# Optimization experiments

Hardware: AMD Instinct MI355X
Metric: run time of the kernel (lower is better)

Reference implementation:

```python
import jax, jax.numpy as jnp
import numpy as np

S_Q = 2048; B = 2; H = 16; D = 128
SCALE = 1.0 / np.sqrt(128.0)  # softmax_scale from init


def setup_inputs() -> dict:
    key = jax.random.key(0)
    kq, kk, kv, ks = jax.random.split(key, 4)
    q = jax.random.normal(kq, (S_Q, B, H, D), dtype=jnp.float32)
    k = jax.random.normal(kk, (S_Q, B, 1, D), dtype=jnp.float32)   # MQA: H_kv=1
    v = jax.random.normal(kv, (S_Q, B, 1, D), dtype=jnp.float32)
    sinks = jax.random.normal(ks, (H,), dtype=jnp.float32)         # learned per-head sink logits
    return {"q": q, "k": k, "v": v, "sinks": sinks, "mask": 0}


def reference(q, k, v, sinks, mask):
    # q: [S_q, B, H, D]; k, v: [S_k, B, H_kv, D] (H_kv may be 1 -> MQA expand)
    S_q, Bn, Hq, Dn = q.shape
    S_k = k.shape[0]
    k = jnp.broadcast_to(k, (S_k, Bn, Hq, Dn))
    v = jnp.broadcast_to(v, (S_k, Bn, Hq, Dn))
    # logits: [B, H, S_q, S_k]
    logits = jnp.einsum("sbhd,tbhd->bhst", q.astype(jnp.float32), k.astype(jnp.float32)) * SCALE
    # causal mask (triu(-inf, diag=1) added in original)
    causal = jnp.tril(jnp.ones((S_q, S_k), dtype=bool))
    logits = jnp.where(causal[None, None], logits, -jnp.inf)
    # sink-augmented softmax: append sink logit as extra column, softmax, drop it
    sink = sinks.astype(jnp.float32)[None, :, None, None]        # [1, H, 1, 1]
    m = jax.lax.stop_gradient(jnp.maximum(logits.max(axis=-1, keepdims=True), sink))
    e = jnp.exp(logits - m)                                      # [B, H, S_q, S_k]
    denom = e.sum(axis=-1, keepdims=True) + jnp.exp(sink - m)    # sink column contribution
    probs = e / denom
    out = jnp.einsum("bhst,tbhd->sbhd", probs.astype(v.dtype), v)  # [S_q, B, H, D]
    return out.reshape(S_q, Bn, Hq * Dn)
```

## Files before the change

kernel.cpp:

```cpp
#include <hip/hip_runtime.h>

#define SQ 2048
#define NB 2
#define NH 16
#define DH 128
#define NKT 32
#define NQT 32
#define SCALE_L2E 0.1275174609f
#define LOG2E 1.4426950408889634f
#define DEFER_THR 11.0f

typedef _Float16 f16x8 __attribute__((ext_vector_type(8)));
typedef _Float16 f16x4 __attribute__((ext_vector_type(4)));
typedef float f32x4 __attribute__((ext_vector_type(4)));

static __device__ __forceinline__ _Float16 f2h(float f) { return (_Float16)f; }

__global__ __launch_bounds__(256)
void prepack(const float* __restrict__ k, const float* __restrict__ v,
             _Float16* __restrict__ kws, _Float16* __restrict__ vws) {
    const int bid   = blockIdx.x;
    const int which = bid >> 6;
    const int b     = (bid >> 5) & 1;
    const int t     = bid & 31;
    const int tid   = threadIdx.x;

    if (which == 0) {
        const float* kbase = k + (size_t)t * 64 * (NB * DH) + b * DH;
        _Float16* dst = kws + ((size_t)b * NKT + t) * 8192;
        #pragma unroll
        for (int p = 0; p < 8; ++p) {
            const int id4 = p * 256 + tid;
            const int row = id4 >> 5;
            const int c0  = (id4 & 31) << 2;
            f32x4 a = *(const f32x4*)(kbase + (size_t)row * (NB * DH) + c0);
            const int e = (row * 128 + c0) ^ ((row & 7) << 3);
            f16x4 pk = { f2h(a.x), f2h(a.y), f2h(a.z), f2h(a.w) };
            *(f16x4*)(dst + e) = pk;
        }
    } else {
        const float* vbase = v + b * DH;
        _Float16* dst = vws + ((size_t)b * NKT + t) * 8192;
        const int d    = tid & 127;
        const int half = tid >> 7;
        #pragma unroll
        for (int p = 0; p < 8; ++p) {
            const int c0 = (p * 2 + half) * 4;
            float a0 = vbase[(size_t)(t * 64 + c0 + 0) * (NB * DH) + d];
            float a1 = vbase[(size_t)(t * 64 + c0 + 1) * (NB * DH) + d];
            float a2 = vbase[(size_t)(t * 64 + c0 + 2) * (NB * DH) + d];
            float a3 = vbase[(size_t)(t * 64 + c0 + 3) * (NB * DH) + d];
            const int e = (d * 64 + c0) ^ ((d & 7) << 3);
            f16x4 pk = { f2h(a0), f2h(a1), f2h(a2), f2h(a3) };
            *(f16x4*)(dst + e) = pk;
        }
    }
}

static __device__ __forceinline__ void gload16(const _Float16* gsrc, _Float16* ldst) {
    __builtin_amdgcn_global_load_lds(
        (const __attribute__((address_space(1))) void*)gsrc,
        (__attribute__((address_space(3))) void*)ldst, 16, 0, 0);
}

static __device__ __forceinline__ void tile_update(
    const _Float16* __restrict__ Kc, const _Float16* __restrict__ Vc,
    _Float16* __restrict__ Pw, const f16x8* __restrict__ qf,
    f32x4* __restrict__ acc, float& m_run, float& l_run,
    int ktb, int sq, int q0w, int r, int g, int lane) {

    float sv[16];
    #pragma unroll
    for (int ct = 0; ct < 4; ++ct) {
        f32x4 sa = (f32x4)(0.0f);
        const int c = ct * 16 + r;
        #pragma unroll
        for (int kc = 0; kc < 4; ++kc) {
            const int e = (c * 128 + kc * 32 + g * 8) ^ ((c & 7) << 3);
            f16x8 kf = *(const f16x8*)(&Kc[e]);
            sa = __builtin_amdgcn_mfma_f32_16x16x32_f16(kf, qf[kc], sa, 0, 0, 0);
        }
        #pragma unroll
        for (int i = 0; i < 4; ++i) sv[ct * 4 + i] = sa[i];
    }

    if (ktb + 63 > q0w) {
        #pragma unroll
        for (int ct = 0; ct < 4; ++ct)
            #pragma unroll
            for (int i = 0; i < 4; ++i) {
                const int tk = ktb + ct * 16 + g * 4 + i;
                if (tk > sq) sv[ct * 4 + i] = -1e30f;
            }
    }

    float m0 = fmaxf(fmaxf(sv[0], sv[1]), fmaxf(sv[2], sv[3]));
    float m1 = fmaxf(fmaxf(sv[4], sv[5]), fmaxf(sv[6], sv[7]));
    float m2 = fmaxf(fmaxf(sv[8], sv[9]), fmaxf(sv[10], sv[11]));
    float m3 = fmaxf(fmaxf(sv[12], sv[13]), fmaxf(sv[14], sv[15]));
    float mx = fmaxf(fmaxf(m0, m1), fmaxf(m2, m3));
    mx = fmaxf(mx, __shfl_xor(mx, 16));
    mx = fmaxf(mx, __shfl_xor(mx, 32));

    if (!__all(mx <= m_run + DEFER_THR)) {
        const float mnew = fmaxf(m_run, mx);
        const float corr = __builtin_amdgcn_exp2f(m_run - mnew);
        m_run = mnew;
        l_run *= corr;
        #pragma unroll
        for (int i = 0; i < 4; ++i) {
            const float ci = __shfl(corr, (lane & 48) | (g * 4 + i));
            #pragma unroll
            for (int nb = 0; nb < 8; ++nb) acc[nb][i] *= ci;
        }
    }

    #pragma unroll
    for (int i = 0; i < 16; ++i)
        sv[i] = __builtin_amdgcn_exp2f(sv[i] - m_run);
    float t0 = (sv[0] + sv[1]) + (sv[2] + sv[3]);
    float t1 = (sv[4] + sv[5]) + (sv[6] + sv[7]);
    float t2 = (sv[8] + sv[9]) + (sv[10] + sv[11]);
    float t3 = (sv[12] + sv[13]) + (sv[14] + sv[15]);
    float ls = (t0 + t1) + (t2 + t3);
    ls += __shfl_xor(ls, 16);
    ls += __shfl_xor(ls, 32);
    l_run += ls;

    #pragma unroll
    for (int ct = 0; ct < 4; ++ct) {
        f16x4 pb = { f2h(sv[ct * 4 + 0]), f2h(sv[ct * 4 + 1]),
                     f2h(sv[ct * 4 + 2]), f2h(sv[ct * 4 + 3]) };
        const int c0 = ct * 16 + g * 4;
        const int e = (r * 64 + c0) ^ ((r & 7) << 3);
        *(f16x4*)(&Pw[e]) = pb;
    }

    #pragma unroll
    for (int cc = 0; cc < 2; ++cc) {
        const int ep = (r * 64 + cc * 32 + g * 8) ^ ((r & 7) << 3);
        f16x8 pf = *(const f16x8*)(&Pw[ep]);
        #pragma unroll
        for (int nb = 0; nb < 8; ++nb) {
            const int d = nb * 16 + r;
            const int ev = (d * 64 + cc * 32 + g * 8) ^ ((d & 7) << 3);
            f16x8 vf = *(const f16x8*)(&Vc[ev]);
            acc[nb] = __builtin_amdgcn_mfma_f32_16x16x32_f16(pf, vf, acc[nb], 0, 0, 0);
        }
    }
}

__global__ __launch_bounds__(256, 2)
void attn_fwd(const float* __restrict__ q, const _Float16* __restrict__ kws,
              const _Float16* __restrict__ vws, const float* __restrict__ sinks,
              float* __restrict__ out) {
    __shared__ _Float16 Kb[2][8192];
    __shared__ _Float16 Vb[2][8192];
    __shared__ _Float16 Plds[4][1024];

    const int tid  = threadIdx.x;
    const int w    = tid >> 6;
    const int lane = tid & 63;
    const int r    = lane & 15;
    const int g    = lane >> 4;

    const int bid = blockIdx.x;
    const int bh  = bid & 31;
    const int b   = bh & 1;
    const int h   = bh >> 1;
    const int j   = bid >> 5;
    const int qtL = j, qtH = NQT - 1 - j;
    const int q0L = qtL * 64, q0H = qtH * 64;
    const int sqL = q0L + w * 16 + r, sqH = q0H + w * 16 + r;

    f16x8 qfL[4], qfH[4];
    #pragma unroll
    for (int ctx = 0; ctx < 2; ++ctx) {
        const int sq = ctx ? sqH : sqL;
        f16x8* qf = ctx ? qfH : qfL;
        const float* qrow = q + ((size_t)sq * NB + b) * (NH * DH) + h * DH;
        #pragma unroll
        for (int kc = 0; kc < 4; ++kc) {
            const int d0 = kc * 32 + g * 8;
            f32x4 a = *(const f32x4*)(qrow + d0);
            f32x4 c = *(const f32x4*)(qrow + d0 + 4);
            f16x8 t;
            t[0] = f2h(a.x * SCALE_L2E); t[1] = f2h(a.y * SCALE_L2E);
            t[2] = f2h(a.z * SCALE_L2E); t[3] = f2h(a.w * SCALE_L2E);
            t[4] = f2h(c.x * SCALE_L2E); t[5] = f2h(c.y * SCALE_L2E);
            t[6] = f2h(c.z * SCALE_L2E); t[7] = f2h(c.w * SCALE_L2E);
            qf[kc] = t;
        }
    }

    const float sink2 = sinks[h] * LOG2E;
    float mL = sink2, lL = 1.0f, mH = sink2, lH = 1.0f;
    f32x4 accL[8], accH[8];
    #pragma unroll
    for (int i = 0; i < 8; ++i) { accL[i] = (f32x4)(0.0f); accH[i] = (f32x4)(0.0f); }

    const _Float16* ktiles = kws + (size_t)b * NKT * 8192;
    const _Float16* vtiles = vws + (size_t)b * NKT * 8192;
    const int ntiles = qtH + 1;

    #pragma unroll
    for (int p = 0; p < 4; ++p) {
        const int off = (p * 256 + tid) * 8;
        gload16(ktiles + off, &Kb[0][off]);
        gload16(vtiles + off, &Vb[0][off]);
    }
    asm volatile("s_waitcnt vmcnt(0)" ::: "memory");
    __builtin_amdgcn_s_barrier();

    for (int it = 0; it < ntiles; ++it) {
        const int cur = it & 1;
        if (it + 1 < ntiles) {
            const _Float16* kn = ktiles + (size_t)(it + 1) * 8192;
            const _Float16* vn = vtiles + (size_t)(it + 1) * 8192;
            #pragma unroll
            for (int p = 0; p < 4; ++p) {
                const int off = (p * 256 + tid) * 8;
                gload16(kn + off, &Kb[cur ^ 1][off]);
                gload16(vn + off, &Vb[cur ^ 1][off]);
            }
        }

        const int ktb = it * 64;
        if (ktb <= q0H + w * 16 + 15)
            tile_update(Kb[cur], Vb[cur], Plds[w], qfH, accH, mH, lH,
                        ktb, sqH, q0H + w * 16, r, g, lane);
        if (ktb <= q0L + w * 16 + 15)
            tile_update(Kb[cur], Vb[cur], Plds[w], qfL, accL, mL, lL,
                        ktb, sqL, q0L + w * 16, r, g, lane);

        asm volatile("s_waitcnt vmcnt(0)" ::: "memory");
        __builtin_amdgcn_s_barrier();
    }

    #pragma unroll
    for (int ctx = 0; ctx < 2; ++ctx) {
        const int q0 = ctx ? q0H : q0L;
        const float lr = ctx ? lH : lL;
        const f32x4* acc = ctx ? accH : accL;
        #pragma unroll
        for (int i = 0; i < 4; ++i) {
            const float li = __shfl(lr, (lane & 48) | (g * 4 + i));
            const float rl = 1.0f / li;
            const int row = q0 + w * 16 + g * 4 + i;
            float* op = out + ((size_t)row * NB + b) * (NH * DH) + h * DH + r;
            #pragma unroll
            for (int nb = 0; nb < 8; ++nb)
                op[nb * 16] = acc[nb][i] * rl;
        }
    }
}

extern "C" void kernel_launch(void* const* d_in, const int* in_sizes, int n_in,
                              void* d_out, int out_size, void* d_ws, size_t ws_size,
                              hipStream_t stream) {
    const float* q     = (const float*)d_in[0];
    const float* k     = (const float*)d_in[1];
    const float* v     = (const float*)d_in[2];
    const float* sinks = (const float*)d_in[3];
    float* out = (float*)d_out;

    _Float16* kws = (_Float16*)d_ws;
    _Float16* vws = kws + (size_t)NB * NKT * 8192;

    prepack<<<dim3(128), 256, 0, stream>>>(k, v, kws, vws);
    attn_fwd<<<dim3((NQT / 2) * NB * NH), 256, 0, stream>>>(q, kws, vws, sinks, out);
}
```

Baseline: 72.60 us.

## Split paired q-tiles into separate blocks and read V directly from global

Each block now handles one 64-row query tile instead of a low/high causal pair, which doubles the grid to 1024 blocks and raises occupancy to 4 blocks per CU. V is no longer staged through LDS: it is prepacked unswizzled and loaded straight from global/L2 into registers before the PV MFMAs, halving LDS use. The row-sum reduction and the sink term are moved out of the loop to the epilogue, and s_setprio is raised around the MFMA sections. The risks are exposed global-load latency for V and the loss of the balanced causal pairing, which is only partly recovered by interleaving tile order.

```diff
diff --git a/kernel.cpp b/kernel.cpp
--- a/kernel.cpp
+++ b/kernel.cpp
@@ -50,7 +50,7 @@
             float a1 = vbase[(size_t)(t * 64 + c0 + 1) * (NB * DH) + d];
             float a2 = vbase[(size_t)(t * 64 + c0 + 2) * (NB * DH) + d];
             float a3 = vbase[(size_t)(t * 64 + c0 + 3) * (NB * DH) + d];
-            const int e = (d * 64 + c0) ^ ((d & 7) << 3);
+            const int e = d * 64 + c0;
             f16x4 pk = { f2h(a0), f2h(a1), f2h(a2), f2h(a3) };
             *(f16x4*)(dst + e) = pk;
         }
@@ -63,99 +63,11 @@
         (__attribute__((address_space(3))) void*)ldst, 16, 0, 0);
 }
 
-static __device__ __forceinline__ void tile_update(
-    const _Float16* __restrict__ Kc, const _Float16* __restrict__ Vc,
-    _Float16* __restrict__ Pw, const f16x8* __restrict__ qf,
-    f32x4* __restrict__ acc, float& m_run, float& l_run,
-    int ktb, int sq, int q0w, int r, int g, int lane) {
-
-    float sv[16];
-    #pragma unroll
-    for (int ct = 0; ct < 4; ++ct) {
-        f32x4 sa = (f32x4)(0.0f);
-        const int c = ct * 16 + r;
-        #pragma unroll
-        for (int kc = 0; kc < 4; ++kc) {
-            const int e = (c * 128 + kc * 32 + g * 8) ^ ((c & 7) << 3);
-            f16x8 kf = *(const f16x8*)(&Kc[e]);
-            sa = __builtin_amdgcn_mfma_f32_16x16x32_f16(kf, qf[kc], sa, 0, 0, 0);
-        }
-        #pragma unroll
-        for (int i = 0; i < 4; ++i) sv[ct * 4 + i] = sa[i];
-    }
-
-    if (ktb + 63 > q0w) {
-        #pragma unroll
-        for (int ct = 0; ct < 4; ++ct)
-            #pragma unroll
-            for (int i = 0; i < 4; ++i) {
-                const int tk = ktb + ct * 16 + g * 4 + i;
-                if (tk > sq) sv[ct * 4 + i] = -1e30f;
-            }
-    }
-
-    float m0 = fmaxf(fmaxf(sv[0], sv[1]), fmaxf(sv[2], sv[3]));
-    float m1 = fmaxf(fmaxf(sv[4], sv[5]), fmaxf(sv[6], sv[7]));
-    float m2 = fmaxf(fmaxf(sv[8], sv[9]), fmaxf(sv[10], sv[11]));
-    float m3 = fmaxf(fmaxf(sv[12], sv[13]), fmaxf(sv[14], sv[15]));
-    float mx = fmaxf(fmaxf(m0, m1), fmaxf(m2, m3));
-    mx = fmaxf(mx, __shfl_xor(mx, 16));
-    mx = fmaxf(mx, __shfl_xor(mx, 32));
-
-    if (!__all(mx <= m_run + DEFER_THR)) {
-        const float mnew = fmaxf(m_run, mx);
-        const float corr = __builtin_amdgcn_exp2f(m_run - mnew);
-        m_run = mnew;
-        l_run *= corr;
-        #pragma unroll
-        for (int i = 0; i < 4; ++i) {
-            const float ci = __shfl(corr, (lane & 48) | (g * 4 + i));
-            #pragma unroll
-            for (int nb = 0; nb < 8; ++nb) acc[nb][i] *= ci;
-        }
-    }
-
-    #pragma unroll
-    for (int i = 0; i < 16; ++i)
-        sv[i] = __builtin_amdgcn_exp2f(sv[i] - m_run);
-    float t0 = (sv[0] + sv[1]) + (sv[2] + sv[3]);
-    float t1 = (sv[4] + sv[5]) + (sv[6] + sv[7]);
-    float t2 = (sv[8] + sv[9]) + (sv[10] + sv[11]);
-    float t3 = (sv[12] + sv[13]) + (sv[14] + sv[15]);
-    float ls = (t0 + t1) + (t2 + t3);
-    ls += __shfl_xor(ls, 16);
-    ls += __shfl_xor(ls, 32);
-    l_run += ls;
-
-    #pragma unroll
-    for (int ct = 0; ct < 4; ++ct) {
-        f16x4 pb = { f2h(sv[ct * 4 + 0]), f2h(sv[ct * 4 + 1]),
-                     f2h(sv[ct * 4 + 2]), f2h(sv[ct * 4 + 3]) };
-        const int c0 = ct * 16 + g * 4;
-        const int e = (r * 64 + c0) ^ ((r & 7) << 3);
-        *(f16x4*)(&Pw[e]) = pb;
-    }
-
-    #pragma unroll
-    for (int cc = 0; cc < 2; ++cc) {
-        const int ep = (r * 64 + cc * 32 + g * 8) ^ ((r & 7) << 3);
-        f16x8 pf = *(const f16x8*)(&Pw[ep]);
-        #pragma unroll
-        for (int nb = 0; nb < 8; ++nb) {
-            const int d = nb * 16 + r;
-            const int ev = (d * 64 + cc * 32 + g * 8) ^ ((d & 7) << 3);
-            f16x8 vf = *(const f16x8*)(&Vc[ev]);
-            acc[nb] = __builtin_amdgcn_mfma_f32_16x16x32_f16(pf, vf, acc[nb], 0, 0, 0);
-        }
-    }
-}
-
-__global__ __launch_bounds__(256, 2)
+__global__ __launch_bounds__(256, 4)
 void attn_fwd(const float* __restrict__ q, const _Float16* __restrict__ kws,
               const _Float16* __restrict__ vws, const float* __restrict__ sinks,
               float* __restrict__ out) {
     __shared__ _Float16 Kb[2][8192];
-    __shared__ _Float16 Vb[2][8192];
     __shared__ _Float16 Plds[4][1024];
 
     const int tid  = threadIdx.x;
@@ -164,20 +76,21 @@
     const int r    = lane & 15;
     const int g    = lane >> 4;
 
-    const int bid = blockIdx.x;
-    const int bh  = bid & 31;
-    const int b   = bh & 1;
-    const int h   = bh >> 1;
-    const int j   = bid >> 5;
-    const int qtL = j, qtH = NQT - 1 - j;
-    const int q0L = qtL * 64, q0H = qtH * 64;
-    const int sqL = q0L + w * 16 + r, sqH = q0H + w * 16 + r;
-
-    f16x8 qfL[4], qfH[4];
-    #pragma unroll
-    for (int ctx = 0; ctx < 2; ++ctx) {
-        const int sq = ctx ? sqH : sqL;
-        f16x8* qf = ctx ? qfH : qfL;
+    const int bid  = blockIdx.x;
+    const int bh   = bid & 31;
+    const int b    = bh & 1;
+    const int h    = bh >> 1;
+    const int slot = bid >> 5;
+    const int jj   = slot & 7;
+    const int mm   = slot >> 3;
+    const int qt = (mm == 0) ? jj : (mm == 1) ? 15 - jj
+                 : (mm == 2) ? 16 + jj : 31 - jj;
+    const int q0  = qt * 64;
+    const int q0w = q0 + w * 16;
+    const int sq  = q0w + r;
+
+    f16x8 qf[4];
+    {
         const float* qrow = q + ((size_t)sq * NB + b) * (NH * DH) + h * DH;
         #pragma unroll
         for (int kc = 0; kc < 4; ++kc) {
@@ -194,20 +107,21 @@
     }
 
     const float sink2 = sinks[h] * LOG2E;
-    float mL = sink2, lL = 1.0f, mH = sink2, lH = 1.0f;
-    f32x4 accL[8], accH[8];
+    float m_run = sink2;
+    float l_p   = 0.0f;
+    f32x4 acc[8];
     #pragma unroll
-    for (int i = 0; i < 8; ++i) { accL[i] = (f32x4)(0.0f); accH[i] = (f32x4)(0.0f); }
+    for (int i = 0; i < 8; ++i) acc[i] = (f32x4)(0.0f);
 
     const _Float16* ktiles = kws + (size_t)b * NKT * 8192;
     const _Float16* vtiles = vws + (size_t)b * NKT * 8192;
-    const int ntiles = qtH + 1;
+    const int ntiles = qt + 1;
+    const int wlimit = q0w + 15;
 
     #pragma unroll
     for (int p = 0; p < 4; ++p) {
         const int off = (p * 256 + tid) * 8;
         gload16(ktiles + off, &Kb[0][off]);
-        gload16(vtiles + off, &Vb[0][off]);
     }
     asm volatile("s_waitcnt vmcnt(0)" ::: "memory");
     __builtin_amdgcn_s_barrier();
@@ -216,42 +130,127 @@
         const int cur = it & 1;
         if (it + 1 < ntiles) {
             const _Float16* kn = ktiles + (size_t)(it + 1) * 8192;
-            const _Float16* vn = vtiles + (size_t)(it + 1) * 8192;
             #pragma unroll
             for (int p = 0; p < 4; ++p) {
                 const int off = (p * 256 + tid) * 8;
                 gload16(kn + off, &Kb[cur ^ 1][off]);
-                gload16(vn + off, &Vb[cur ^ 1][off]);
             }
         }
 
         const int ktb = it * 64;
-        if (ktb <= q0H + w * 16 + 15)
-            tile_update(Kb[cur], Vb[cur], Plds[w], qfH, accH, mH, lH,
-                        ktb, sqH, q0H + w * 16, r, g, lane);
-        if (ktb <= q0L + w * 16 + 15)
-            tile_update(Kb[cur], Vb[cur], Plds[w], qfL, accL, mL, lL,
-                        ktb, sqL, q0L + w * 16, r, g, lane);
+        if (ktb <= wlimit) {
+            float sv[16];
+            __builtin_amdgcn_s_setprio(1);
+            #pragma unroll
+            for (int ct = 0; ct < 4; ++ct) {
+                f32x4 sa = (f32x4)(0.0f);
+                const int c = ct * 16 + r;
+                #pragma unroll
+                for (int kc = 0; kc < 4; ++kc) {
+                    const int e = (c * 128 + kc * 32 + g * 8) ^ ((c & 7) << 3);
+                    f16x8 kf = *(const f16x8*)(&Kb[cur][e]);
+                    sa = __builtin_amdgcn_mfma_f32_16x16x32_f16(kf, qf[kc], sa, 0, 0, 0);
+                }
+                #pragma unroll
+                for (int i = 0; i < 4; ++i) sv[ct * 4 + i] = sa[i];
+            }
+            __builtin_amdgcn_s_setprio(0);
+
+            if (ktb + 63 > q0w) {
+                #pragma unroll
+                for (int ct = 0; ct < 4; ++ct)
+                    #pragma unroll
+                    for (int i = 0; i < 4; ++i) {
+                        const int tk = ktb + ct * 16 + g * 4 + i;
+                        if (tk > sq) sv[ct * 4 + i] = -1e30f;
+                    }
+            }
+
+            float m0 = fmaxf(fmaxf(sv[0], sv[1]), fmaxf(sv[2], sv[3]));
+            float m1 = fmaxf(fmaxf(sv[4], sv[5]), fmaxf(sv[6], sv[7]));
+            float m2 = fmaxf(fmaxf(sv[8], sv[9]), fmaxf(sv[10], sv[11]));
+            float m3 = fmaxf(fmaxf(sv[12], sv[13]), fmaxf(sv[14], sv[15]));
+            float mx = fmaxf(fmaxf(m0, m1), fmaxf(m2, m3));
+
+            if (!__all(mx <= m_run + DEFER_THR)) {
+                mx = fmaxf(mx, __shfl_xor(mx, 16));
+                mx = fmaxf(mx, __shfl_xor(mx, 32));
+                const float mnew = fmaxf(m_run, mx);
+                const float corr = __builtin_amdgcn_exp2f(m_run - mnew);
+                m_run = mnew;
+                l_p *= corr;
+                #pragma unroll
+                for (int i = 0; i < 4; ++i) {
+                    const float ci = __shfl(corr, (lane & 48) | (g * 4 + i));
+                    #pragma unroll
+                    for (int nb = 0; nb < 8; ++nb) acc[nb][i] *= ci;
+                }
+            }
+
+            #pragma unroll
+            for (int i = 0; i < 16; ++i)
+                sv[i] = __builtin_amdgcn_exp2f(sv[i] - m_run);
+            float t0 = (sv[0] + sv[1]) + (sv[2] + sv[3]);
+            float t1 = (sv[4] + sv[5]) + (sv[6] + sv[7]);
+            float t2 = (sv[8] + sv[9]) + (sv[10] + sv[11]);
+            float t3 = (sv[12] + sv[13]) + (sv[14] + sv[15]);
+            l_p += (t0 + t1) + (t2 + t3);
+
+            #pragma unroll
+            for (int ct = 0; ct < 4; ++ct) {
+                f16x4 pb = { f2h(sv[ct * 4 + 0]), f2h(sv[ct * 4 + 1]),
+                             f2h(sv[ct * 4 + 2]), f2h(sv[ct * 4 + 3]) };
+                const int c0 = ct * 16 + g * 4;
+                const int e = (r * 64 + c0) ^ ((r & 7) << 3);
+                *(f16x4*)(&Plds[w][e]) = pb;
+            }
+
+            const _Float16* vt = vtiles + (size_t)it * 8192;
+            f16x8 vf[8];
+            #pragma unroll
+            for (int nb = 0; nb < 8; ++nb)
+                vf[nb] = *(const f16x8*)(vt + (nb * 16 + r) * 64 + g * 8);
+            {
+                const int ep = (r * 64 + g * 8) ^ ((r & 7) << 3);
+                f16x8 pf = *(const f16x8*)(&Plds[w][ep]);
+                __builtin_amdgcn_s_setprio(1);
+                #pragma unroll
+                for (int nb = 0; nb < 8; ++nb)
+                    acc[nb] = __builtin_amdgcn_mfma_f32_16x16x32_f16(pf, vf[nb], acc[nb], 0, 0, 0);
+                __builtin_amdgcn_s_setprio(0);
+            }
+            #pragma unroll
+            for (int nb = 0; nb < 8; ++nb)
+                vf[nb] = *(const f16x8*)(vt + (nb * 16 + r) * 64 + 32 + g * 8);
+            {
+                const int ep = (r * 64 + 32 + g * 8) ^ ((r & 7) << 3);
+                f16x8 pf = *(const f16x8*)(&Plds[w][ep]);
+                __builtin_amdgcn_s_setprio(1);
+                #pragma unroll
+                for (int nb = 0; nb < 8; ++nb)
+                    acc[nb] = __builtin_amdgcn_mfma_f32_16x16x32_f16(pf, vf[nb], acc[nb], 0, 0, 0);
+                __builtin_amdgcn_s_setprio(0);
+            }
+        }
 
         asm volatile("s_waitcnt vmcnt(0)" ::: "memory");
         __builtin_amdgcn_s_barrier();
     }
 
+    float ls = l_p;
+    ls += __shfl_xor(ls, 16);
+    ls += __shfl_xor(ls, 32);
     #pragma unroll
-    for (int ctx = 0; ctx < 2; ++ctx) {
-        const int q0 = ctx ? q0H : q0L;
-        const float lr = ctx ? lH : lL;
-        const f32x4* acc = ctx ? accH : accL;
-        #pragma unroll
-        for (int i = 0; i < 4; ++i) {
-            const float li = __shfl(lr, (lane & 48) | (g * 4 + i));
-            const float rl = 1.0f / li;
-            const int row = q0 + w * 16 + g * 4 + i;
-            float* op = out + ((size_t)row * NB + b) * (NH * DH) + h * DH + r;
-            #pragma unroll
-            for (int nb = 0; nb < 8; ++nb)
-                op[nb * 16] = acc[nb][i] * rl;
-        }
+    for (int i = 0; i < 4; ++i) {
+        const int sel = (lane & 48) | (g * 4 + i);
+        const float mi = __shfl(m_run, sel);
+        const float li = __shfl(ls, sel) + __builtin_amdgcn_exp2f(sink2 - mi);
+        const float rl = 1.0f / li;
+        const int row = q0 + w * 16 + g * 4 + i;
+        float* op = out + ((size_t)row * NB + b) * (NH * DH) + h * DH + r;
+        #pragma unroll
+        for (int nb = 0; nb < 8; ++nb)
+            op[nb * 16] = acc[nb][i] * rl;
     }
 }
 
@@ -268,5 +267,5 @@
     _Float16* vws = kws + (size_t)NB * NKT * 8192;
 
     prepack<<<dim3(128), 256, 0, stream>>>(k, v, kws, vws);
-    attn_fwd<<<dim3((NQT / 2) * NB * NH), 256, 0, stream>>>(q, kws, vws, sinks, out);
-}
+    attn_fwd<<<dim3(NQT * NB * NH), 256, 0, stream>>>(q, kws, vws, sinks, out);
+}
```

Measured after the change: 159.1 us. +119.1%, slower.

## Interleave low/high query tiles to share K/V LDS fragments and raise MFMA priority

Applied to the files above, without the earlier changes.

When both the low and high query tiles are active, the QK^T and PV loops now process them together, so each K and V fragment read from LDS feeds two MFMAs. This interleaves independent MFMA chains. The per-wave P scratch buffer is doubled so both tiles' probabilities can be staged at once. s_setprio raises wave priority around the MFMA sections. The cost is higher register pressure from two live score arrays, which may cause spills under the (256,2) launch bounds.

```diff
diff --git a/kernel.cpp b/kernel.cpp
--- a/kernel.cpp
+++ b/kernel.cpp
@@ -63,36 +63,10 @@
         (__attribute__((address_space(3))) void*)ldst, 16, 0, 0);
 }
 
-static __device__ __forceinline__ void tile_update(
-    const _Float16* __restrict__ Kc, const _Float16* __restrict__ Vc,
-    _Float16* __restrict__ Pw, const f16x8* __restrict__ qf,
-    f32x4* __restrict__ acc, float& m_run, float& l_run,
-    int ktb, int sq, int q0w, int r, int g, int lane) {
-
-    float sv[16];
-    #pragma unroll
-    for (int ct = 0; ct < 4; ++ct) {
-        f32x4 sa = (f32x4)(0.0f);
-        const int c = ct * 16 + r;
-        #pragma unroll
-        for (int kc = 0; kc < 4; ++kc) {
-            const int e = (c * 128 + kc * 32 + g * 8) ^ ((c & 7) << 3);
-            f16x8 kf = *(const f16x8*)(&Kc[e]);
-            sa = __builtin_amdgcn_mfma_f32_16x16x32_f16(kf, qf[kc], sa, 0, 0, 0);
-        }
-        #pragma unroll
-        for (int i = 0; i < 4; ++i) sv[ct * 4 + i] = sa[i];
-    }
-
-    if (ktb + 63 > q0w) {
-        #pragma unroll
-        for (int ct = 0; ct < 4; ++ct)
-            #pragma unroll
-            for (int i = 0; i < 4; ++i) {
-                const int tk = ktb + ct * 16 + g * 4 + i;
-                if (tk > sq) sv[ct * 4 + i] = -1e30f;
-            }
-    }
+static __device__ __forceinline__ void softmax_pv(
+    const _Float16* __restrict__ Vc, _Float16* __restrict__ Pw,
+    float* __restrict__ sv, f32x4* __restrict__ acc,
+    float& m_run, float& l_run, int r, int g, int lane) {
 
     float m0 = fmaxf(fmaxf(sv[0], sv[1]), fmaxf(sv[2], sv[3]));
     float m1 = fmaxf(fmaxf(sv[4], sv[5]), fmaxf(sv[6], sv[7]));
@@ -140,6 +114,7 @@
     for (int cc = 0; cc < 2; ++cc) {
         const int ep = (r * 64 + cc * 32 + g * 8) ^ ((r & 7) << 3);
         f16x8 pf = *(const f16x8*)(&Pw[ep]);
+        __builtin_amdgcn_s_setprio(1);
         #pragma unroll
         for (int nb = 0; nb < 8; ++nb) {
             const int d = nb * 16 + r;
@@ -147,6 +122,7 @@
             f16x8 vf = *(const f16x8*)(&Vc[ev]);
             acc[nb] = __builtin_amdgcn_mfma_f32_16x16x32_f16(pf, vf, acc[nb], 0, 0, 0);
         }
+        __builtin_amdgcn_s_setprio(0);
     }
 }
 
@@ -156,7 +132,7 @@
               float* __restrict__ out) {
     __shared__ _Float16 Kb[2][8192];
     __shared__ _Float16 Vb[2][8192];
-    __shared__ _Float16 Plds[4][1024];
+    __shared__ _Float16 Plds[4][2][1024];
 
     const int tid  = threadIdx.x;
     const int w    = tid >> 6;
@@ -211,6 +187,7 @@
     }
     asm volatile("s_waitcnt vmcnt(0)" ::: "memory");
     __builtin_amdgcn_s_barrier();
+    asm volatile("" ::: "memory");
 
     for (int it = 0; it < ntiles; ++it) {
         const int cur = it & 1;
@@ -226,15 +203,172 @@
         }
 
         const int ktb = it * 64;
-        if (ktb <= q0H + w * 16 + 15)
-            tile_update(Kb[cur], Vb[cur], Plds[w], qfH, accH, mH, lH,
-                        ktb, sqH, q0H + w * 16, r, g, lane);
-        if (ktb <= q0L + w * 16 + 15)
-            tile_update(Kb[cur], Vb[cur], Plds[w], qfL, accL, mL, lL,
-                        ktb, sqL, q0L + w * 16, r, g, lane);
+        const bool aliveL = (ktb <= q0L + w * 16 + 15);
+
+        if (aliveL) {
+            float svL[16], svH[16];
+            __builtin_amdgcn_s_setprio(1);
+            #pragma unroll
+            for (int ct = 0; ct < 4; ++ct) {
+                f32x4 saL = (f32x4)(0.0f), saH = (f32x4)(0.0f);
+                const int c = ct * 16 + r;
+                #pragma unroll
+                for (int kc = 0; kc < 4; ++kc) {
+                    const int e = (c * 128 + kc * 32 + g * 8) ^ ((c & 7) << 3);
+                    f16x8 kf = *(const f16x8*)(&Kb[cur][e]);
+                    saL = __builtin_amdgcn_mfma_f32_16x16x32_f16(kf, qfL[kc], saL, 0, 0, 0);
+                    saH = __builtin_amdgcn_mfma_f32_16x16x32_f16(kf, qfH[kc], saH, 0, 0, 0);
+                }
+                #pragma unroll
+                for (int i = 0; i < 4; ++i) { svL[ct * 4 + i] = saL[i]; svH[ct * 4 + i] = saH[i]; }
+            }
+            __builtin_amdgcn_s_setprio(0);
+
+            if (ktb + 63 > q0L + w * 16) {
+                #pragma unroll
+                for (int ct = 0; ct < 4; ++ct)
+                    #pragma unroll
+                    for (int i = 0; i < 4; ++i) {
+                        const int tk = ktb + ct * 16 + g * 4 + i;
+                        if (tk > sqL) svL[ct * 4 + i] = -1e30f;
+                    }
+            }
+            if (ktb + 63 > q0H + w * 16) {
+                #pragma unroll
+                for (int ct = 0; ct < 4; ++ct)
+                    #pragma unroll
+                    for (int i = 0; i < 4; ++i) {
+                        const int tk = ktb + ct * 16 + g * 4 + i;
+                        if (tk > sqH) svH[ct * 4 + i] = -1e30f;
+                    }
+            }
+
+            softmax_pv_prep:;
+            {
+                float m0 = fmaxf(fmaxf(svL[0], svL[1]), fmaxf(svL[2], svL[3]));
+                float m1 = fmaxf(fmaxf(svL[4], svL[5]), fmaxf(svL[6], svL[7]));
+                float m2 = fmaxf(fmaxf(svL[8], svL[9]), fmaxf(svL[10], svL[11]));
+                float m3 = fmaxf(fmaxf(svL[12], svL[13]), fmaxf(svL[14], svL[15]));
+                float mx = fmaxf(fmaxf(m0, m1), fmaxf(m2, m3));
+                mx = fmaxf(mx, __shfl_xor(mx, 16));
+                mx = fmaxf(mx, __shfl_xor(mx, 32));
+                if (!__all(mx <= mL + DEFER_THR)) {
+                    const float mnew = fmaxf(mL, mx);
+                    const float corr = __builtin_amdgcn_exp2f(mL - mnew);
+                    mL = mnew; lL *= corr;
+                    #pragma unroll
+                    for (int i = 0; i < 4; ++i) {
+                        const float ci = __shfl(corr, (lane & 48) | (g * 4 + i));
+                        #pragma unroll
+                        for (int nb = 0; nb < 8; ++nb) accL[nb][i] *= ci;
+                    }
+                }
+                #pragma unroll
+                for (int i = 0; i < 16; ++i) svL[i] = __builtin_amdgcn_exp2f(svL[i] - mL);
+                float t0 = (svL[0] + svL[1]) + (svL[2] + svL[3]);
+                float t1 = (svL[4] + svL[5]) + (svL[6] + svL[7]);
+                float t2 = (svL[8] + svL[9]) + (svL[10] + svL[11]);
+                float t3 = (svL[12] + svL[13]) + (svL[14] + svL[15]);
+                float ls = (t0 + t1) + (t2 + t3);
+                ls += __shfl_xor(ls, 16);
+                ls += __shfl_xor(ls, 32);
+                lL += ls;
+                #pragma unroll
+                for (int ct = 0; ct < 4; ++ct) {
+                    f16x4 pb = { f2h(svL[ct * 4 + 0]), f2h(svL[ct * 4 + 1]),
+                                 f2h(svL[ct * 4 + 2]), f2h(svL[ct * 4 + 3]) };
+                    const int e = (r * 64 + ct * 16 + g * 4) ^ ((r & 7) << 3);
+                    *(f16x4*)(&Plds[w][0][e]) = pb;
+                }
+            }
+            {
+                float m0 = fmaxf(fmaxf(svH[0], svH[1]), fmaxf(svH[2], svH[3]));
+                float m1 = fmaxf(fmaxf(svH[4], svH[5]), fmaxf(svH[6], svH[7]));
+                float m2 = fmaxf(fmaxf(svH[8], svH[9]), fmaxf(svH[10], svH[11]));
+                float m3 = fmaxf(fmaxf(svH[12], svH[13]), fmaxf(svH[14], svH[15]));
+                float mx = fmaxf(fmaxf(m0, m1), fmaxf(m2, m3));
+                mx = fmaxf(mx, __shfl_xor(mx, 16));
+                mx = fmaxf(mx, __shfl_xor(mx, 32));
+                if (!__all(mx <= mH + DEFER_THR)) {
+                    const float mnew = fmaxf(mH, mx);
+                    const float corr = __builtin_amdgcn_exp2f(mH - mnew);
+                    mH = mnew; lH *= corr;
+                    #pragma unroll
+                    for (int i = 0; i < 4; ++i) {
+                        const float ci = __shfl(corr, (lane & 48) | (g * 4 + i));
+                        #pragma unroll
+                        for (int nb = 0; nb < 8; ++nb) accH[nb][i] *= ci;
+                    }
+                }
+                #pragma unroll
+                for (int i = 0; i < 16; ++i) svH[i] = __builtin_amdgcn_exp2f(svH[i] - mH);
+                float t0 = (svH[0] + svH[1]) + (svH[2] + svH[3]);
+                float t1 = (svH[4] + svH[5]) + (svH[6] + svH[7]);
+                float t2 = (svH[8] + svH[9]) + (svH[10] + svH[11]);
+                float t3 = (svH[12] + svH[13]) + (svH[14] + svH[15]);
+                float ls = (t0 + t1) + (t2 + t3);
+                ls += __shfl_xor(ls, 16);
+                ls += __shfl_xor(ls, 32);
+                lH += ls;
+                #pragma unroll
+                for (int ct = 0; ct < 4; ++ct) {
+                    f16x4 pb = { f2h(svH[ct * 4 + 0]), f2h(svH[ct * 4 + 1]),
+                                 f2h(svH[ct * 4 + 2]), f2h(svH[ct * 4 + 3]) };
+                    const int e = (r * 64 + ct * 16 + g * 4) ^ ((r & 7) << 3);
+                    *(f16x4*)(&Plds[w][1][e]) = pb;
+                }
+            }
+
+            #pragma unroll
+            for (int cc = 0; cc < 2; ++cc) {
+                const int ep = (r * 64 + cc * 32 + g * 8) ^ ((r & 7) << 3);
+                f16x8 pfL = *(const f16x8*)(&Plds[w][0][ep]);
+                f16x8 pfH = *(const f16x8*)(&Plds[w][1][ep]);
+                __builtin_amdgcn_s_setprio(1);
+                #pragma unroll
+                for (int nb = 0; nb < 8; ++nb) {
+                    const int d = nb * 16 + r;
+                    const int ev = (d * 64 + cc * 32 + g * 8) ^ ((d & 7) << 3);
+                    f16x8 vf = *(const f16x8*)(&Vb[cur][ev]);
+                    accL[nb] = __builtin_amdgcn_mfma_f32_16x16x32_f16(pfL, vf, accL[nb], 0, 0, 0);
+                    accH[nb] = __builtin_amdgcn_mfma_f32_16x16x32_f16(pfH, vf, accH[nb], 0, 0, 0);
+                }
+                __builtin_amdgcn_s_setprio(0);
+            }
+        } else {
+            float svH[16];
+            __builtin_amdgcn_s_setprio(1);
+            #pragma unroll
+            for (int ct = 0; ct < 4; ++ct) {
+                f32x4 sa = (f32x4)(0.0f);
+                const int c = ct * 16 + r;
+                #pragma unroll
+                for (int kc = 0; kc < 4; ++kc) {
+                    const int e = (c * 128 + kc * 32 + g * 8) ^ ((c & 7) << 3);
+                    f16x8 kf = *(const f16x8*)(&Kb[cur][e]);
+                    sa = __builtin_amdgcn_mfma_f32_16x16x32_f16(kf, qfH[kc], sa, 0, 0, 0);
+                }
+                #pragma unroll
+                for (int i = 0; i < 4; ++i) svH[ct * 4 + i] = sa[i];
+            }
+            __builtin_amdgcn_s_setprio(0);
+
+            if (ktb + 63 > q0H + w * 16) {
+                #pragma unroll
+                for (int ct = 0; ct < 4; ++ct)
+                    #pragma unroll
+                    for (int i = 0; i < 4; ++i) {
+                        const int tk = ktb + ct * 16 + g * 4 + i;
+                        if (tk > sqH) svH[ct * 4 + i] = -1e30f;
+                    }
+            }
+
+            softmax_pv(Vb[cur], Plds[w][1], svH, accH, mH, lH, r, g, lane);
+        }
 
         asm volatile("s_waitcnt vmcnt(0)" ::: "memory");
         __builtin_amdgcn_s_barrier();
+        asm volatile("" ::: "memory");
     }
 
     #pragma unroll
```

Measured after the change: 72.84 us. Within noise of the previous version (+0.3%).
